# Kernel optimization log

Hardware: AMD Instinct MI355X
Metric: run time of the kernel (lower is better)

## Reference

```python
import jax, jax.numpy as jnp
import numpy as np
from jax import lax

D_MODEL = 1024
N_HEADS = 16
D_HEAD = 64
INNER = N_HEADS * D_HEAD
EPS = 1e-12  # F.normalize eps


def setup_inputs() -> dict:
    key = jax.random.key(0)
    ks = jax.random.split(key, 7)
    B, T = 4, 2048
    s = 1.0 / np.sqrt(D_MODEL)
    return {
        "x": jax.random.normal(ks[0], (B, T, D_MODEL), dtype=jnp.float32),
        "Wq": jax.random.normal(ks[1], (D_MODEL, INNER), dtype=jnp.float32) * s,
        "Wk": jax.random.normal(ks[2], (D_MODEL, INNER), dtype=jnp.float32) * s,
        "Wv": jax.random.normal(ks[3], (D_MODEL, INNER), dtype=jnp.float32) * s,
        "Wbeta": jax.random.normal(ks[4], (D_MODEL, N_HEADS), dtype=jnp.float32) * s,
        "b_beta": jax.random.normal(ks[5], (N_HEADS,), dtype=jnp.float32) * 0.01,
        "Wout": jax.random.normal(ks[6], (INNER, D_MODEL), dtype=jnp.float32) * (1.0 / np.sqrt(INNER)),
    }


def _delta_net(x, Wq, Wk, Wv, Wbeta, b_beta, Wout):
    B, T, _ = x.shape
    H, D = N_HEADS, D_HEAD
    Q = (x @ Wq).reshape(B, T, H, D)
    K = (x @ Wk).reshape(B, T, H, D)
    V = (x @ Wv).reshape(B, T, H, D)
    beta = jax.nn.sigmoid(x @ Wbeta + b_beta)  # (B,T,H)
    # L2-normalize keys along head dim (torch F.normalize semantics)
    K = K / jnp.maximum(jnp.linalg.norm(K, axis=-1, keepdims=True), EPS)

    # time-major for scan: (T,B,H,D) and (T,B,H)
    xs = (
        jnp.moveaxis(Q, 1, 0),
        jnp.moveaxis(K, 1, 0),
        jnp.moveaxis(V, 1, 0),
        jnp.moveaxis(beta, 1, 0),
    )

    def step(W, inp):
        q_t, k_t, v_t, b_t = inp
        pred = jnp.einsum('bhij,bhj->bhi', W, k_t)
        err = v_t - pred
        W_new = W + b_t[..., None, None] * jnp.einsum('bhi,bhj->bhij', err, k_t)
        o_t = jnp.einsum('bhij,bhj->bhi', W_new, q_t)
        return W_new, o_t

    W0 = jnp.zeros((B, H, D, D), dtype=x.dtype)
    _, O = lax.scan(step, W0, xs)  # O: (T,B,H,D)
    out = jnp.moveaxis(O, 0, 1).reshape(B, T, H * D)
    return out @ Wout


def reference(x, Wq, Wk, Wv, Wbeta, b_beta, Wout):
    return _delta_net(x, Wq, Wk, Wv, Wbeta, b_beta, Wout)
```

## Files before the change

### kernel.cpp

```cpp
#include <hip/hip_runtime.h>
#include <hip/hip_bf16.h>

#define BATCH 4
#define TSEQ 2048
#define DM 1024
#define NH 16
#define DH 64
#define MROWS (BATCH * TSEQ)
#define CHUNK 64
#define NCHUNK (TSEQ / CHUNK)

typedef __attribute__((ext_vector_type(8))) short bf16x8;
typedef __attribute__((ext_vector_type(4))) float f32x4;

#define GLOAD16(g, l)                                                        \
    __builtin_amdgcn_global_load_lds(                                        \
        (const __attribute__((address_space(1))) void*)(g),                  \
        (__attribute__((address_space(3))) void*)(l), 16, 0, 0)

__device__ __forceinline__ float ldf(const float* p) { return *p; }
__device__ __forceinline__ float ldf(const __hip_bfloat16* p) { return __bfloat162float(*p); }
__device__ __forceinline__ void stf(float* p, float v) { *p = v; }
__device__ __forceinline__ void stf(__hip_bfloat16* p, float v) { *p = __float2bfloat16(v); }

__device__ __forceinline__ int swz(int row, int cb) {
    return row * 128 + (cb ^ ((row & 7) << 4));
}
__device__ __forceinline__ bf16x8 ldfrag(const __hip_bfloat16* b, int rowblk, int kf, int lane) {
    const int row = rowblk * 16 + (lane & 15);
    const int cb = kf * 64 + ((lane >> 4) << 4);
    return *(const bf16x8*)((const char*)b + swz(row, cb));
}
__device__ __forceinline__ unsigned short bfbits(float f) {
    __hip_bfloat16 h = __float2bfloat16(f);
    return *(unsigned short*)&h;
}

template <int NSPLIT>
__global__ __launch_bounds__(256) void gemm_mfma(const __hip_bfloat16* __restrict__ Ah,
                                                 const __hip_bfloat16* __restrict__ BT,
                                                 float* __restrict__ Cf,
                                                 __hip_bfloat16* __restrict__ Qh,
                                                 int M, int N, int K) {
    __shared__ __align__(16) __hip_bfloat16 As[128 * 64];
    __shared__ __align__(16) __hip_bfloat16 Bs[128 * 64];
    const int tid = threadIdx.x;
    const int wave = tid >> 6;
    const int lane = tid & 63;
    const int wr = wave >> 1;
    const int wc = wave & 1;

    const int gx = gridDim.x;
    const int nwg = gx * gridDim.y;
    int bid = blockIdx.y * gx + blockIdx.x;
    bid = (bid & 7) * (nwg >> 3) + (bid >> 3);
    const int bx = bid % gx;
    const int by = bid / gx;
    const int wsel = (NSPLIT > 1) ? (bx >> 3) : 0;
    const __hip_bfloat16* BTp = BT + (size_t)wsel * DM * DM;
    const int rowBase = by * 128;
    const int colBase = ((NSPLIT > 1) ? (bx & 7) : bx) * 128;

    f32x4 acc[4][4] = {};

    const size_t Kz = (size_t)K;
    const int sg = (lane & 7) ^ (lane >> 3);
    const int rw0 = wave * 8 + (lane >> 3);

    for (int k0 = 0; k0 < K; k0 += 64) {
#pragma unroll
        for (int i = 0; i < 4; ++i) {
            const int row = rw0 + i * 32;
            GLOAD16(Ah + ((size_t)(rowBase + row) * Kz + k0 + sg * 8),
                    (char*)As + wave * 1024 + i * 4096);
            GLOAD16(BTp + ((size_t)(colBase + row) * Kz + k0 + sg * 8),
                    (char*)Bs + wave * 1024 + i * 4096);
        }
        __syncthreads();

#pragma unroll
        for (int kf = 0; kf < 2; ++kf) {
            bf16x8 af[4], bfr[4];
#pragma unroll
            for (int i = 0; i < 4; ++i) {
                const int ra = wr * 64 + i * 16 + (lane & 15);
                const int rb = wc * 64 + i * 16 + (lane & 15);
                const int slot = kf * 4 + (lane >> 4);
                const int cba = (slot ^ (lane & 7)) << 4;
                af[i] = *(const bf16x8*)((const char*)As + ra * 128 + cba);
                bfr[i] = *(const bf16x8*)((const char*)Bs + rb * 128 + cba);
            }
#pragma unroll
            for (int mi = 0; mi < 4; ++mi)
#pragma unroll
                for (int ni = 0; ni < 4; ++ni)
                    acc[mi][ni] = __builtin_amdgcn_mfma_f32_16x16x32_bf16(af[mi], bfr[ni],
                                                                          acc[mi][ni], 0, 0, 0);
        }
        __syncthreads();
    }

    if (NSPLIT > 1 && wsel == 0) {
#pragma unroll
        for (int mi = 0; mi < 4; ++mi)
#pragma unroll
            for (int ni = 0; ni < 4; ++ni) {
                const int col = colBase + wc * 64 + ni * 16 + (lane & 15);
#pragma unroll
                for (int r = 0; r < 4; ++r) {
                    const int row = rowBase + wr * 64 + mi * 16 + (lane >> 4) * 4 + r;
                    Qh[(size_t)row * N + col] = __float2bfloat16(acc[mi][ni][r]);
                }
            }
    } else {
        float* Cp = (NSPLIT > 1) ? (Cf + (size_t)(wsel - 1) * ((size_t)M * N)) : Cf;
#pragma unroll
        for (int mi = 0; mi < 4; ++mi)
#pragma unroll
            for (int ni = 0; ni < 4; ++ni) {
                const int col = colBase + wc * 64 + ni * 16 + (lane & 15);
#pragma unroll
                for (int r = 0; r < 4; ++r) {
                    const int row = rowBase + wr * 64 + mi * 16 + (lane >> 4) * 4 + r;
                    Cp[(size_t)row * N + col] = acc[mi][ni][r];
                }
            }
    }
}

__global__ __launch_bounds__(256) void conv_bf16(const float* __restrict__ in,
                                                 __hip_bfloat16* __restrict__ out, int n8) {
    const int i = blockIdx.x * 256 + threadIdx.x;
    if (i >= n8) return;
    const float4* p = (const float4*)in + (size_t)i * 2;
    float4 a = p[0], b = p[1];
    __hip_bfloat16 t[8] = {__float2bfloat16(a.x), __float2bfloat16(a.y),
                           __float2bfloat16(a.z), __float2bfloat16(a.w),
                           __float2bfloat16(b.x), __float2bfloat16(b.y),
                           __float2bfloat16(b.z), __float2bfloat16(b.w)};
    *(uint4*)(out + (size_t)i * 8) = *(const uint4*)t;
}

__global__ __launch_bounds__(256) void convT_bf16(const float* __restrict__ W,
                                                  __hip_bfloat16* __restrict__ WT) {
    __shared__ __hip_bfloat16 tile[64][65];
    const int tid = threadIdx.x;
    const int c = tid & 63;
    const int r4 = tid >> 6;
    const int kb = blockIdx.y * 64;
    const int nb = blockIdx.x * 64;
#pragma unroll
    for (int i = 0; i < 16; ++i) {
        const int r = r4 + i * 4;
        tile[r][c] = __float2bfloat16(W[(size_t)(kb + r) * DM + nb + c]);
    }
    __syncthreads();
#pragma unroll
    for (int i = 0; i < 16; ++i) {
        const int r = r4 + i * 4;
        WT[(size_t)(nb + r) * DM + kb + c] = tile[c][r];
    }
}

__global__ __launch_bounds__(256) void beta_kernel(const float* __restrict__ x,
                                                   const float* __restrict__ Wb,
                                                   const float* __restrict__ bb,
                                                   float* __restrict__ beta) {
    const int tid = threadIdx.x;
    const int h = tid % NH;
    const int rl = tid / NH;
    const int row = blockIdx.x * 16 + rl;
    const float* xr = x + (size_t)row * DM;
    float acc = 0.f;
#pragma unroll 8
    for (int k = 0; k < DM; ++k) acc += xr[k] * Wb[k * NH + h];
    acc += bb[h];
    beta[row * NH + h] = 1.f / (1.f + __expf(-acc));
}

__global__ __launch_bounds__(256) void delta_prepass(const float* __restrict__ K,
                                                     float* __restrict__ V,
                                                     const float* __restrict__ beta,
                                                     __hip_bfloat16* __restrict__ Wtt,
                                                     __hip_bfloat16* __restrict__ Kntt,
                                                     __hip_bfloat16* __restrict__ Knh) {
    const int chunk = blockIdx.x;
    const int bh = blockIdx.y;
    const int b = bh >> 4;
    const int h = bh & 15;
    const int tid = threadIdx.x;
    const int wave = tid >> 6;
    const int lane = tid & 63;
    const int lt = tid >> 2;
    const int j0 = (tid & 3) * 16;
    const int c0 = chunk * CHUNK;
    const size_t tileIdx = (size_t)bh * NCHUNK + chunk;

    __shared__ __align__(16) char smem_raw[17408 + 33792];
    float (*Am2)[68] = reinterpret_cast<float(*)[68]>(smem_raw);
    __hip_bfloat16* Knb = reinterpret_cast<__hip_bfloat16*>(smem_raw + 17408);
    float (*RT)[66] = reinterpret_cast<float(*)[66]>(smem_raw + 17408);
    __shared__ float sbeta[CHUNK];

    const size_t gstride = NH * DH;
    const size_t gbase = (size_t)b * TSEQ * gstride + (size_t)h * DH;
    const float* kp = K + gbase + (size_t)(c0 + lt) * gstride + j0;
    float* vp = V + gbase + (size_t)(c0 + lt) * gstride + j0;

    float4 k0 = ((const float4*)kp)[0];
    float4 k1 = ((const float4*)kp)[1];
    float4 k2 = ((const float4*)kp)[2];
    float4 k3 = ((const float4*)kp)[3];
    float ss = k0.x * k0.x + k0.y * k0.y + k0.z * k0.z + k0.w * k0.w +
               k1.x * k1.x + k1.y * k1.y + k1.z * k1.z + k1.w * k1.w +
               k2.x * k2.x + k2.y * k2.y + k2.z * k2.z + k2.w * k2.w +
               k3.x * k3.x + k3.y * k3.y + k3.z * k3.z + k3.w * k3.w;
    ss += __shfl_xor(ss, 1);
    ss += __shfl_xor(ss, 2);
    const float rn = 1.f / fmaxf(sqrtf(ss), 1e-12f);
    k0.x *= rn; k0.y *= rn; k0.z *= rn; k0.w *= rn;
    k1.x *= rn; k1.y *= rn; k1.z *= rn; k1.w *= rn;
    k2.x *= rn; k2.y *= rn; k2.z *= rn; k2.w *= rn;
    k3.x *= rn; k3.y *= rn; k3.z *= rn; k3.w *= rn;

    {
        __hip_bfloat16 t[16];
        const float kk[16] = {k0.x, k0.y, k0.z, k0.w, k1.x, k1.y, k1.z, k1.w,
                              k2.x, k2.y, k2.z, k2.w, k3.x, k3.y, k3.z, k3.w};
#pragma unroll
        for (int e = 0; e < 16; ++e) t[e] = __float2bfloat16(kk[e]);
        *(uint4*)((char*)Knb + swz(lt, j0 * 2)) = *(const uint4*)&t[0];
        *(uint4*)((char*)Knb + swz(lt, j0 * 2 + 16)) = *(const uint4*)&t[8];
        __hip_bfloat16* knh = Knh + gbase + (size_t)(c0 + lt) * gstride + j0;
        *(uint4*)knh = *(const uint4*)&t[0];
        *(uint4*)(knh + 8) = *(const uint4*)&t[8];
    }

    float4 v0 = ((const float4*)vp)[0];
    float4 v1 = ((const float4*)vp)[1];
    float4 v2 = ((const float4*)vp)[2];
    float4 v3 = ((const float4*)vp)[3];

    if (tid < CHUNK)
        sbeta[tid] = beta[((size_t)(b * TSEQ + c0 + tid)) * NH + h];
    __syncthreads();

    {
        f32x4 accA[4] = {};
#pragma unroll
        for (int kf = 0; kf < 2; ++kf) {
            bf16x8 ka = ldfrag(Knb, wave, kf, lane);
#pragma unroll
            for (int sb = 0; sb < 4; ++sb)
                accA[sb] = __builtin_amdgcn_mfma_f32_16x16x32_bf16(
                    ka, ldfrag(Knb, sb, kf, lane), accA[sb], 0, 0, 0);
        }
        float bt[4];
#pragma unroll
        for (int r = 0; r < 4; ++r) bt[r] = sbeta[16 * wave + (lane >> 4) * 4 + r];
#pragma unroll
        for (int sb = 0; sb < 4; ++sb)
#pragma unroll
            for (int r = 0; r < 4; ++r) {
                const int row = 16 * wave + (lane >> 4) * 4 + r;
                const int s = 16 * sb + (lane & 15);
                Am2[row][s] = (s < row) ? bt[r] * accA[sb][r] : 0.f;
            }
    }
    __syncthreads();

    {
        const int jr = tid >> 2;
        const int tq = (tid & 3) * 16;
        unsigned short pk[16];
#pragma unroll
        for (int i = 0; i < 16; ++i)
            pk[i] = *(const unsigned short*)((const char*)Knb + swz(tq + i, jr * 2));
        char* kt = (char*)Kntt + tileIdx * 8192;
        *(uint4*)(kt + swz(jr, tq * 2)) = *(const uint4*)&pk[0];
        *(uint4*)(kt + swz(jr, tq * 2 + 16)) = *(const uint4*)&pk[8];
    }
    __syncthreads();

    {
        const float bl = sbeta[lt];
        float vv[16] = {v0.x, v0.y, v0.z, v0.w, v1.x, v1.y, v1.z, v1.w,
                        v2.x, v2.y, v2.z, v2.w, v3.x, v3.y, v3.z, v3.w};
        float kk[16] = {k0.x, k0.y, k0.z, k0.w, k1.x, k1.y, k1.z, k1.w,
                        k2.x, k2.y, k2.z, k2.w, k3.x, k3.y, k3.z, k3.w};
#pragma unroll
        for (int e = 0; e < 16; ++e) {
            RT[j0 + e][lt] = bl * vv[e];
            RT[64 + j0 + e][lt] = bl * kk[e];
        }
    }
    __syncthreads();

    {
        const int c = tid >> 1;
        const int hh = tid & 1;
        float2 ra[16];
#pragma unroll
        for (int lp = 0; lp < 16; ++lp)
            ra[lp] = *(const float2*)&RT[c][4 * lp + 2 * hh];

#pragma unroll
        for (int tt = 0; tt < 16; ++tt) {
            const int t = 4 * tt;
            float2 mine = ra[tt];
            float2 other;
            other.x = __shfl_xor(mine.x, 1);
            other.y = __shfl_xor(mine.y, 1);
            const float r0 = hh ? other.x : mine.x;
            const float r1 = hh ? other.y : mine.y;
            const float r2 = hh ? mine.x : other.x;
            const float r3 = hh ? mine.y : other.y;
            const float4 q1 = *(const float4*)&Am2[t + 1][t];
            const float4 q2 = *(const float4*)&Am2[t + 2][t];
            const float4 q3 = *(const float4*)&Am2[t + 3][t];
            const float p0 = r0;
            const float p1 = r1 - q1.x * p0;
            const float p2 = r2 - q2.x * p0 - q2.y * p1;
            const float p3 = r3 - q3.x * p0 - q3.y * p1 - q3.z * p2;
            ra[tt] = hh ? make_float2(p2, p3) : make_float2(p0, p1);
#pragma unroll
            for (int lp = tt + 1; lp < 16; ++lp) {
                const int pr = 4 * lp + 2 * hh;
                const float4 ca = *(const float4*)&Am2[pr][t];
                const float4 cb = *(const float4*)&Am2[pr + 1][t];
                ra[lp].x -= ca.x * p0 + ca.y * p1 + ca.z * p2 + ca.w * p3;
                ra[lp].y -= cb.x * p0 + cb.y * p1 + cb.z * p2 + cb.w * p3;
            }
        }
#pragma unroll
        for (int lp = 0; lp < 16; ++lp)
            *(float2*)&RT[c][4 * lp + 2 * hh] = ra[lp];
    }
    __syncthreads();

    {
        float uu[16], ww[16];
#pragma unroll
        for (int e = 0; e < 16; ++e) {
            uu[e] = RT[j0 + e][lt];
            ww[e] = RT[64 + j0 + e][lt];
        }
#pragma unroll
        for (int q = 0; q < 4; ++q)
            ((float4*)vp)[q] = make_float4(uu[q * 4 + 0], uu[q * 4 + 1], uu[q * 4 + 2], uu[q * 4 + 3]);
        __hip_bfloat16 tw[16];
#pragma unroll
        for (int e = 0; e < 16; ++e) tw[e] = __float2bfloat16(ww[e]);
        char* wt = (char*)Wtt + tileIdx * 8192;
        *(uint4*)(wt + swz(lt, j0 * 2)) = *(const uint4*)&tw[0];
        *(uint4*)(wt + swz(lt, j0 * 2 + 16)) = *(const uint4*)&tw[8];
    }
}

__global__ __launch_bounds__(256) void scan_thin(const float* __restrict__ Ug,
                                                 const __hip_bfloat16* __restrict__ Wt,
                                                 const __hip_bfloat16* __restrict__ Kt,
                                                 __hip_bfloat16* __restrict__ Sg,
                                                 __hip_bfloat16* __restrict__ Utg) {
    const int bh = blockIdx.x;
    const int b = bh >> 4;
    const int h = bh & 15;
    const int tid = threadIdx.x;
    const int wave = tid >> 6;
    const int lane = tid & 63;
    const int srow = tid >> 2;
    const int sj0 = (tid & 3) * 16;

    __shared__ __align__(16) __hip_bfloat16 wb[2][64 * 64];
    __shared__ __align__(16) __hip_bfloat16 knT[2][64 * 64];
    __shared__ __align__(16) __hip_bfloat16 Sb[64 * 64];
    __shared__ __align__(16) __hip_bfloat16 Ut[64 * 64];

    const size_t gstride = NH * DH;
    const size_t gbase = (size_t)b * TSEQ * gstride + (size_t)h * DH;
    const size_t tileBase = (size_t)bh * NCHUNK;

    auto stage_tiles = [&](int buf, int c) {
        const char* wsrc = (const char*)Wt + (tileBase + c) * 8192 + wave * 1024 + lane * 16;
        const char* ksrc = (const char*)Kt + (tileBase + c) * 8192 + wave * 1024 + lane * 16;
#pragma unroll
        for (int q = 0; q < 2; ++q) {
            GLOAD16(wsrc + q * 4096, (char*)wb[buf] + wave * 1024 + q * 4096);
            GLOAD16(ksrc + q * 4096, (char*)knT[buf] + wave * 1024 + q * 4096);
        }
    };

    for (int i = tid; i < 512; i += 256) ((uint4*)Sb)[i] = make_uint4(0, 0, 0, 0);
    stage_tiles(0, 0);

    float up[4][4];
#pragma unroll
    for (int ib = 0; ib < 4; ++ib)
#pragma unroll
        for (int r = 0; r < 4; ++r) {
            const int t = 16 * wave + (lane >> 4) * 4 + r;
            up[ib][r] = Ug[gbase + (size_t)t * gstride + 16 * ib + (lane & 15)];
        }

    f32x4 Sreg[4] = {};
    __syncthreads();

    for (int c = 0; c < NCHUNK; ++c) {
        const int cur = c & 1;

        {
            uint4 a = *(const uint4*)((const char*)Sb + swz(srow, sj0 * 2));
            uint4 a2 = *(const uint4*)((const char*)Sb + swz(srow, sj0 * 2 + 16));
            __hip_bfloat16* gp = Sg + (tileBase + c) * 4096 + srow * 64 + sj0;
            *(uint4*)gp = a;
            *(uint4*)(gp + 8) = a2;
        }
        f32x4 accU[4] = {};
#pragma unroll
        for (int f = 0; f < 2; ++f) {
            bf16x8 wa = ldfrag(wb[cur], wave, f, lane);
#pragma unroll
            for (int ib = 0; ib < 4; ++ib)
                accU[ib] = __builtin_amdgcn_mfma_f32_16x16x32_bf16(
                    wa, ldfrag(Sb, ib, f, lane), accU[ib], 0, 0, 0);
        }
#pragma unroll
        for (int ib = 0; ib < 4; ++ib) {
            unsigned short pk[4];
#pragma unroll
            for (int r = 0; r < 4; ++r) pk[r] = bfbits(up[ib][r] - accU[ib][r]);
            const int irow = 16 * ib + (lane & 15);
            const int tcb = (16 * wave + (lane >> 4) * 4) * 2;
            *(unsigned long long*)((char*)Ut + swz(irow, tcb)) = *(const unsigned long long*)pk;
        }
        __syncthreads();

#pragma unroll
        for (int f = 0; f < 2; ++f) {
            bf16x8 ua = ldfrag(Ut, wave, f, lane);
#pragma unroll
            for (int jb = 0; jb < 4; ++jb)
                Sreg[jb] = __builtin_amdgcn_mfma_f32_16x16x32_bf16(
                    ua, ldfrag(knT[cur], jb, f, lane), Sreg[jb], 0, 0, 0);
        }
        {
            uint4 a = *(const uint4*)((const char*)Ut + swz(srow, sj0 * 2));
            uint4 a2 = *(const uint4*)((const char*)Ut + swz(srow, sj0 * 2 + 16));
            __hip_bfloat16* gp = Utg + (tileBase + c) * 4096 + srow * 64 + sj0;
            *(uint4*)gp = a;
            *(uint4*)(gp + 8) = a2;
        }
#pragma unroll
        for (int jb = 0; jb < 4; ++jb)
#pragma unroll
            for (int r = 0; r < 4; ++r) {
                const int irow = 16 * wave + (lane >> 4) * 4 + r;
                const int j = 16 * jb + (lane & 15);
                *(unsigned short*)((char*)Sb + swz(irow, j * 2)) = bfbits(Sreg[jb][r]);
            }
        if (c + 1 < NCHUNK) {
            stage_tiles(cur ^ 1, c + 1);
            const size_t nOff = (size_t)((c + 1) * CHUNK);
#pragma unroll
            for (int ib = 0; ib < 4; ++ib)
#pragma unroll
                for (int r = 0; r < 4; ++r) {
                    const int t = 16 * wave + (lane >> 4) * 4 + r;
                    up[ib][r] = Ug[gbase + (nOff + t) * gstride + 16 * ib + (lane & 15)];
                }
        }
        __syncthreads();
    }
}

__global__ __launch_bounds__(256) void delta_output(const __hip_bfloat16* __restrict__ Qh,
                                                    const __hip_bfloat16* __restrict__ Knh,
                                                    const __hip_bfloat16* __restrict__ Sg,
                                                    const __hip_bfloat16* __restrict__ Utg,
                                                    __hip_bfloat16* __restrict__ Ohg) {
    const int c = blockIdx.x;
    const int bh = blockIdx.y;
    const int b = bh >> 4;
    const int h = bh & 15;
    const int tid = threadIdx.x;
    const int wave = tid >> 6;
    const int lane = tid & 63;
    const int srow = tid >> 2;
    const int sj0 = (tid & 3) * 16;

    __shared__ __align__(16) __hip_bfloat16 Qb[64 * 64];
    __shared__ __align__(16) __hip_bfloat16 Knb[64 * 64];
    __shared__ __align__(16) __hip_bfloat16 Sbs[64 * 64];
    __shared__ __align__(16) __hip_bfloat16 Utb[64 * 64];
    __shared__ __align__(16) __hip_bfloat16 SSb[64 * 64];

    const size_t gstride = NH * DH;
    const size_t gbase = (size_t)b * TSEQ * gstride + (size_t)h * DH;
    const size_t cOff = (size_t)(c * CHUNK);
    const size_t tile = ((size_t)bh * NCHUNK + c) * 4096;

    {
        const uint4* qp = (const uint4*)(Qh + gbase + (cOff + srow) * gstride + sj0);
        const uint4* kp = (const uint4*)(Knh + gbase + (cOff + srow) * gstride + sj0);
        *(uint4*)((char*)Qb + swz(srow, sj0 * 2)) = qp[0];
        *(uint4*)((char*)Qb + swz(srow, sj0 * 2 + 16)) = qp[1];
        *(uint4*)((char*)Knb + swz(srow, sj0 * 2)) = kp[0];
        *(uint4*)((char*)Knb + swz(srow, sj0 * 2 + 16)) = kp[1];
        const uint4* sp = (const uint4*)(Sg + tile + srow * 64 + sj0);
        const uint4* upp = (const uint4*)(Utg + tile + srow * 64 + sj0);
        *(uint4*)((char*)Sbs + swz(srow, sj0 * 2)) = sp[0];
        *(uint4*)((char*)Sbs + swz(srow, sj0 * 2 + 16)) = sp[1];
        *(uint4*)((char*)Utb + swz(srow, sj0 * 2)) = upp[0];
        *(uint4*)((char*)Utb + swz(srow, sj0 * 2 + 16)) = upp[1];
    }
    __syncthreads();

    f32x4 ss[4] = {};
    f32x4 accO[4] = {};
#pragma unroll
    for (int f = 0; f < 2; ++f) {
        bf16x8 qa = ldfrag(Qb, wave, f, lane);
#pragma unroll
        for (int sb = 0; sb < 4; ++sb)
            ss[sb] = __builtin_amdgcn_mfma_f32_16x16x32_bf16(
                qa, ldfrag(Knb, sb, f, lane), ss[sb], 0, 0, 0);
#pragma unroll
        for (int ib = 0; ib < 4; ++ib)
            accO[ib] = __builtin_amdgcn_mfma_f32_16x16x32_bf16(
                qa, ldfrag(Sbs, ib, f, lane), accO[ib], 0, 0, 0);
    }
#pragma unroll
    for (int sb = 0; sb < 4; ++sb)
#pragma unroll
        for (int r = 0; r < 4; ++r) {
            const int t = 16 * wave + (lane >> 4) * 4 + r;
            const int s = 16 * sb + (lane & 15);
            const float v = (t >= s) ? ss[sb][r] : 0.f;
            *(unsigned short*)((char*)SSb + swz(t, s * 2)) = bfbits(v);
        }
    __syncthreads();

#pragma unroll
    for (int f = 0; f < 2; ++f) {
        bf16x8 sa = ldfrag(SSb, wave, f, lane);
#pragma unroll
        for (int ib = 0; ib < 4; ++ib)
            accO[ib] = __builtin_amdgcn_mfma_f32_16x16x32_bf16(
                sa, ldfrag(Utb, ib, f, lane), accO[ib], 0, 0, 0);
    }
#pragma unroll
    for (int ib = 0; ib < 4; ++ib)
#pragma unroll
        for (int r = 0; r < 4; ++r) {
            const int t = 16 * wave + (lane >> 4) * 4 + r;
            const int i = 16 * ib + (lane & 15);
            Ohg[gbase + (cOff + t) * gstride + i] = __float2bfloat16(accO[ib][r]);
        }
}

#define BM 64
#define BN 64
#define BK 16

template <typename TA, typename TC>
__global__ __launch_bounds__(256) void gemm_kernel(const TA* __restrict__ A,
                                                   const float* __restrict__ B,
                                                   TC* __restrict__ C,
                                                   int M, int N, int K) {
    __shared__ float As[BK][BM + 1];
    __shared__ float Bs[BK][BN + 1];
    const int tid = threadIdx.x;
    const int tr = tid / 16;
    const int tc = tid % 16;
    const int rowBase = blockIdx.y * BM;
    const int colBase = blockIdx.x * BN;

    float acc[4][4];
#pragma unroll
    for (int m = 0; m < 4; ++m)
#pragma unroll
        for (int n = 0; n < 4; ++n) acc[m][n] = 0.f;

    for (int k0 = 0; k0 < K; k0 += BK) {
#pragma unroll
        for (int i = tid; i < BM * BK; i += 256) {
            int r = i / BK, c = i % BK;
            As[c][r] = ldf(&A[(size_t)(rowBase + r) * K + k0 + c]);
        }
#pragma unroll
        for (int i = tid; i < BK * BN; i += 256) {
            int r = i / BN, c = i % BN;
            Bs[r][c] = B[(size_t)(k0 + r) * N + colBase + c];
        }
        __syncthreads();
#pragma unroll
        for (int kk = 0; kk < BK; ++kk) {
            float a[4], b[4];
#pragma unroll
            for (int m = 0; m < 4; ++m) a[m] = As[kk][tr * 4 + m];
#pragma unroll
            for (int n = 0; n < 4; ++n) b[n] = Bs[kk][tc * 4 + n];
#pragma unroll
            for (int m = 0; m < 4; ++m)
#pragma unroll
                for (int n = 0; n < 4; ++n) acc[m][n] += a[m] * b[n];
        }
        __syncthreads();
    }
#pragma unroll
    for (int m = 0; m < 4; ++m)
#pragma unroll
        for (int n = 0; n < 4; ++n)
            stf(&C[(size_t)(rowBase + tr * 4 + m) * N + colBase + tc * 4 + n], acc[m][n]);
}

template <typename TS>
__global__ __launch_bounds__(64) void scan_kernel(const TS* __restrict__ Q,
                                                  const TS* __restrict__ K,
                                                  const TS* __restrict__ V,
                                                  const float* __restrict__ beta,
                                                  float* __restrict__ O) {
    const int bh = blockIdx.x;
    const int b = bh >> 4;
    const int h = bh & 15;
    const int lane = threadIdx.x;

    float Wrow[64];
#pragma unroll
    for (int j = 0; j < 64; ++j) Wrow[j] = 0.f;

    __shared__ float sk[64];
    __shared__ float sq[64];

    size_t base = ((size_t)b * TSEQ) * (NH * DH) + h * DH + lane;
    int brow = b * TSEQ;

    for (int t = 0; t < TSEQ; ++t, base += NH * DH) {
        float k = ldf(&K[base]);
        float q = ldf(&Q[base]);
        float v = ldf(&V[base]);
        float be = beta[(size_t)(brow + t) * NH + h];

        float ss = k * k;
#pragma unroll
        for (int off = 32; off > 0; off >>= 1) ss += __shfl_xor(ss, off);
        k = k / fmaxf(sqrtf(ss), 1e-12f);

        sk[lane] = k;
        sq[lane] = q;
        __syncthreads();

        float p0 = 0.f, p1 = 0.f, p2 = 0.f, p3 = 0.f;
#pragma unroll
        for (int j = 0; j < 64; j += 4) {
            p0 += Wrow[j + 0] * sk[j + 0];
            p1 += Wrow[j + 1] * sk[j + 1];
            p2 += Wrow[j + 2] * sk[j + 2];
            p3 += Wrow[j + 3] * sk[j + 3];
        }
        const float bei = be * (v - ((p0 + p1) + (p2 + p3)));

        float o0 = 0.f, o1 = 0.f, o2 = 0.f, o3 = 0.f;
#pragma unroll
        for (int j = 0; j < 64; j += 4) {
            Wrow[j + 0] += bei * sk[j + 0]; o0 += Wrow[j + 0] * sq[j + 0];
            Wrow[j + 1] += bei * sk[j + 1]; o1 += Wrow[j + 1] * sq[j + 1];
            Wrow[j + 2] += bei * sk[j + 2]; o2 += Wrow[j + 2] * sq[j + 2];
            Wrow[j + 3] += bei * sk[j + 3]; o3 += Wrow[j + 3] * sq[j + 3];
        }
        O[base] = (o0 + o1) + (o2 + o3);
        __syncthreads();
    }
}

extern "C" void kernel_launch(void* const* d_in, const int* in_sizes, int n_in,
                              void* d_out, int out_size, void* d_ws, size_t ws_size,
                              hipStream_t stream) {
    const float* x     = (const float*)d_in[0];
    const float* Wq    = (const float*)d_in[1];
    const float* Wk    = (const float*)d_in[2];
    const float* Wv    = (const float*)d_in[3];
    const float* Wbeta = (const float*)d_in[4];
    const float* bbeta = (const float*)d_in[5];
    const float* Wout  = (const float*)d_in[6];
    float* out = (float*)d_out;

    const size_t projElems = (size_t)MROWS * DM;
    const size_t betaBytes = (size_t)MROWS * NH * 4;
    const size_t f32Bytes  = projElems * 4;
    const size_t bf16Bytes = projElems * 2;
    const size_t need_f32  = 4 * f32Bytes + betaBytes;

    char* ws = (char*)d_ws;
    size_t off = 0;
    auto alloc = [&](size_t bytes) {
        char* p = ws + off;
        off += (bytes + 255) & ~(size_t)255;
        return (void*)p;
    };

    if (ws_size >= need_f32) {
        float* Qf = (float*)alloc(f32Bytes);
        float* Kf = (float*)alloc(f32Bytes);
        float* Vf = (float*)alloc(f32Bytes);
        float* Wmf = (float*)alloc(f32Bytes);
        float* betaf = (float*)alloc(betaBytes);

        __hip_bfloat16* Qh  = (__hip_bfloat16*)Qf;
        __hip_bfloat16* Knh = (__hip_bfloat16*)((char*)Qf + bf16Bytes);

        __hip_bfloat16* xh  = (__hip_bfloat16*)Wmf;
        __hip_bfloat16* WqT = (__hip_bfloat16*)((char*)Wmf + bf16Bytes);
        __hip_bfloat16* WkT = WqT + (size_t)DM * DM;
        __hip_bfloat16* WvT = WkT + (size_t)DM * DM;

        const int n8 = (int)(projElems / 8);
        conv_bf16<<<dim3(n8 / 256), dim3(256), 0, stream>>>(x, xh, n8);
        convT_bf16<<<dim3(16, 16), dim3(256), 0, stream>>>(Wq, WqT);
        convT_bf16<<<dim3(16, 16), dim3(256), 0, stream>>>(Wk, WkT);
        convT_bf16<<<dim3(16, 16), dim3(256), 0, stream>>>(Wv, WvT);

        gemm_mfma<3><<<dim3(24, MROWS / 128), dim3(256), 0, stream>>>(xh, WqT, Kf, Qh,
                                                                      MROWS, DM, DM);
        beta_kernel<<<dim3(MROWS / 16), dim3(256), 0, stream>>>(x, Wbeta, bbeta, betaf);

        __hip_bfloat16* Wtt  = (__hip_bfloat16*)Wmf;
        __hip_bfloat16* Kntt = (__hip_bfloat16*)((char*)Wmf + bf16Bytes);
        delta_prepass<<<dim3(NCHUNK, BATCH * NH), dim3(256), 0, stream>>>(Kf, Vf, betaf,
                                                                          Wtt, Kntt, Knh);

        __hip_bfloat16* Sg  = (__hip_bfloat16*)d_out;
        __hip_bfloat16* Utg = Sg + (size_t)BATCH * NH * NCHUNK * 4096;
        scan_thin<<<dim3(BATCH * NH), dim3(256), 0, stream>>>(Vf, Wtt, Kntt, Sg, Utg);

        __hip_bfloat16* WoutT = (__hip_bfloat16*)Vf;
        __hip_bfloat16* Oh    = (__hip_bfloat16*)Wmf;
        convT_bf16<<<dim3(16, 16), dim3(256), 0, stream>>>(Wout, WoutT);
        delta_output<<<dim3(NCHUNK, BATCH * NH), dim3(256), 0, stream>>>(Qh, Knh, Sg, Utg, Oh);
        gemm_mfma<1><<<dim3(8, MROWS / 128), dim3(256), 0, stream>>>(Oh, WoutT, out, nullptr,
                                                                     MROWS, DM, DM);
    } else {
        __hip_bfloat16* Qh = (__hip_bfloat16*)alloc(bf16Bytes);
        __hip_bfloat16* Kh = (__hip_bfloat16*)alloc(bf16Bytes);
        __hip_bfloat16* Vh = (__hip_bfloat16*)alloc(bf16Bytes);
        float* betaf = (float*)alloc(betaBytes);
        float* Of = (float*)alloc(f32Bytes);

        const dim3 gemmGrid(DM / BN, MROWS / BM);
        gemm_kernel<float, __hip_bfloat16><<<gemmGrid, dim3(256), 0, stream>>>(x, Wq, Qh, MROWS, DM, DM);
        gemm_kernel<float, __hip_bfloat16><<<gemmGrid, dim3(256), 0, stream>>>(x, Wk, Kh, MROWS, DM, DM);
        gemm_kernel<float, __hip_bfloat16><<<gemmGrid, dim3(256), 0, stream>>>(x, Wv, Vh, MROWS, DM, DM);
        beta_kernel<<<dim3(MROWS / 16), dim3(256), 0, stream>>>(x, Wbeta, bbeta, betaf);
        scan_kernel<__hip_bfloat16><<<dim3(BATCH * NH), dim3(64), 0, stream>>>(Qh, Kh, Vh, betaf, Of);
        gemm_kernel<float, float><<<gemmGrid, dim3(256), 0, stream>>>(Of, Wout, out, MROWS, DM, DM);
    }
}
```

Before: 264.2 us.

## Fuse key L2-normalization into QKV GEMM epilogue and store K,V as bf16

The QKV GEMM epilogue now L2-normalizes K rows, using shuffle reductions across the 64-column head tile, and writes Q, normalized K and V directly as bf16 instead of writing K and V as fp32. The prepass reads bf16 K/V, no longer normalizes or re-emits K, and writes the updated U back as bf16. The scan reads U in bf16. This roughly halves the intermediate traffic for K, V and U and removes a redundant K write, at the cost of extra bf16 rounding of V and U before the scan.

```diff
diff --git a/kernel.cpp b/kernel.cpp
--- a/kernel.cpp
+++ b/kernel.cpp
@@ -40,7 +40,8 @@
 __global__ __launch_bounds__(256) void gemm_mfma(const __hip_bfloat16* __restrict__ Ah,
                                                  const __hip_bfloat16* __restrict__ BT,
                                                  float* __restrict__ Cf,
-                                                 __hip_bfloat16* __restrict__ Qh,
+                                                 __hip_bfloat16* __restrict__ QhBase,
+                                                 __hip_bfloat16* __restrict__ Vh,
                                                  int M, int N, int K) {
     __shared__ __align__(16) __hip_bfloat16 As[128 * 64];
     __shared__ __align__(16) __hip_bfloat16 Bs[128 * 64];
@@ -100,7 +101,25 @@
         __syncthreads();
     }
 
-    if (NSPLIT > 1 && wsel == 0) {
+    if (NSPLIT > 1) {
+        if (wsel == 1) {
+#pragma unroll
+            for (int mi = 0; mi < 4; ++mi)
+#pragma unroll
+                for (int r = 0; r < 4; ++r) {
+                    float ss = 0.f;
+#pragma unroll
+                    for (int ni = 0; ni < 4; ++ni) ss += acc[mi][ni][r] * acc[mi][ni][r];
+                    ss += __shfl_xor(ss, 1);
+                    ss += __shfl_xor(ss, 2);
+                    ss += __shfl_xor(ss, 4);
+                    ss += __shfl_xor(ss, 8);
+                    const float rn = 1.f / fmaxf(sqrtf(ss), 1e-12f);
+#pragma unroll
+                    for (int ni = 0; ni < 4; ++ni) acc[mi][ni][r] *= rn;
+                }
+        }
+        __hip_bfloat16* Op = (wsel == 2) ? Vh : (QhBase + (size_t)wsel * ((size_t)M * N));
 #pragma unroll
         for (int mi = 0; mi < 4; ++mi)
 #pragma unroll
@@ -109,11 +128,10 @@
 #pragma unroll
                 for (int r = 0; r < 4; ++r) {
                     const int row = rowBase + wr * 64 + mi * 16 + (lane >> 4) * 4 + r;
-                    Qh[(size_t)row * N + col] = __float2bfloat16(acc[mi][ni][r]);
+                    Op[(size_t)row * N + col] = __float2bfloat16(acc[mi][ni][r]);
                 }
             }
     } else {
-        float* Cp = (NSPLIT > 1) ? (Cf + (size_t)(wsel - 1) * ((size_t)M * N)) : Cf;
 #pragma unroll
         for (int mi = 0; mi < 4; ++mi)
 #pragma unroll
@@ -122,7 +140,7 @@
 #pragma unroll
                 for (int r = 0; r < 4; ++r) {
                     const int row = rowBase + wr * 64 + mi * 16 + (lane >> 4) * 4 + r;
-                    Cp[(size_t)row * N + col] = acc[mi][ni][r];
+                    Cf[(size_t)row * N + col] = acc[mi][ni][r];
                 }
             }
     }
@@ -178,12 +196,11 @@
     beta[row * NH + h] = 1.f / (1.f + __expf(-acc));
 }
 
-__global__ __launch_bounds__(256) void delta_prepass(const float* __restrict__ K,
-                                                     float* __restrict__ V,
+__global__ __launch_bounds__(256) void delta_prepass(const __hip_bfloat16* __restrict__ Knh,
+                                                     __hip_bfloat16* __restrict__ Vh,
                                                      const float* __restrict__ beta,
                                                      __hip_bfloat16* __restrict__ Wtt,
-                                                     __hip_bfloat16* __restrict__ Kntt,
-                                                     __hip_bfloat16* __restrict__ Knh) {
+                                                     __hip_bfloat16* __restrict__ Kntt) {
     const int chunk = blockIdx.x;
     const int bh = blockIdx.y;
     const int b = bh >> 4;
@@ -204,42 +221,30 @@
 
     const size_t gstride = NH * DH;
     const size_t gbase = (size_t)b * TSEQ * gstride + (size_t)h * DH;
-    const float* kp = K + gbase + (size_t)(c0 + lt) * gstride + j0;
-    float* vp = V + gbase + (size_t)(c0 + lt) * gstride + j0;
-
-    float4 k0 = ((const float4*)kp)[0];
-    float4 k1 = ((const float4*)kp)[1];
-    float4 k2 = ((const float4*)kp)[2];
-    float4 k3 = ((const float4*)kp)[3];
-    float ss = k0.x * k0.x + k0.y * k0.y + k0.z * k0.z + k0.w * k0.w +
-               k1.x * k1.x + k1.y * k1.y + k1.z * k1.z + k1.w * k1.w +
-               k2.x * k2.x + k2.y * k2.y + k2.z * k2.z + k2.w * k2.w +
-               k3.x * k3.x + k3.y * k3.y + k3.z * k3.z + k3.w * k3.w;
-    ss += __shfl_xor(ss, 1);
-    ss += __shfl_xor(ss, 2);
-    const float rn = 1.f / fmaxf(sqrtf(ss), 1e-12f);
-    k0.x *= rn; k0.y *= rn; k0.z *= rn; k0.w *= rn;
-    k1.x *= rn; k1.y *= rn; k1.z *= rn; k1.w *= rn;
-    k2.x *= rn; k2.y *= rn; k2.z *= rn; k2.w *= rn;
-    k3.x *= rn; k3.y *= rn; k3.z *= rn; k3.w *= rn;
-
+    const __hip_bfloat16* kp = Knh + gbase + (size_t)(c0 + lt) * gstride + j0;
+    __hip_bfloat16* vp = Vh + gbase + (size_t)(c0 + lt) * gstride + j0;
+
+    const uint4 kraw0 = ((const uint4*)kp)[0];
+    const uint4 kraw1 = ((const uint4*)kp)[1];
+    *(uint4*)((char*)Knb + swz(lt, j0 * 2)) = kraw0;
+    *(uint4*)((char*)Knb + swz(lt, j0 * 2 + 16)) = kraw1;
+    float kk[16], vv[16];
     {
-        __hip_bfloat16 t[16];
-        const float kk[16] = {k0.x, k0.y, k0.z, k0.w, k1.x, k1.y, k1.z, k1.w,
-                              k2.x, k2.y, k2.z, k2.w, k3.x, k3.y, k3.z, k3.w};
-#pragma unroll
-        for (int e = 0; e < 16; ++e) t[e] = __float2bfloat16(kk[e]);
-        *(uint4*)((char*)Knb + swz(lt, j0 * 2)) = *(const uint4*)&t[0];
-        *(uint4*)((char*)Knb + swz(lt, j0 * 2 + 16)) = *(const uint4*)&t[8];
-        __hip_bfloat16* knh = Knh + gbase + (size_t)(c0 + lt) * gstride + j0;
-        *(uint4*)knh = *(const uint4*)&t[0];
-        *(uint4*)(knh + 8) = *(const uint4*)&t[8];
-    }
-
-    float4 v0 = ((const float4*)vp)[0];
-    float4 v1 = ((const float4*)vp)[1];
-    float4 v2 = ((const float4*)vp)[2];
-    float4 v3 = ((const float4*)vp)[3];
+        const __hip_bfloat16* kb16 = (const __hip_bfloat16*)&kraw0;
+#pragma unroll
+        for (int e = 0; e < 8; ++e) kk[e] = __bfloat162float(kb16[e]);
+        kb16 = (const __hip_bfloat16*)&kraw1;
+#pragma unroll
+        for (int e = 0; e < 8; ++e) kk[8 + e] = __bfloat162float(kb16[e]);
+        const uint4 vraw0 = ((const uint4*)vp)[0];
+        const uint4 vraw1 = ((const uint4*)vp)[1];
+        const __hip_bfloat16* vb16 = (const __hip_bfloat16*)&vraw0;
+#pragma unroll
+        for (int e = 0; e < 8; ++e) vv[e] = __bfloat162float(vb16[e]);
+        vb16 = (const __hip_bfloat16*)&vraw1;
+#pragma unroll
+        for (int e = 0; e < 8; ++e) vv[8 + e] = __bfloat162float(vb16[e]);
+    }
 
     if (tid < CHUNK)
         sbeta[tid] = beta[((size_t)(b * TSEQ + c0 + tid)) * NH + h];
@@ -284,10 +289,6 @@
 
     {
         const float bl = sbeta[lt];
-        float vv[16] = {v0.x, v0.y, v0.z, v0.w, v1.x, v1.y, v1.z, v1.w,
-                        v2.x, v2.y, v2.z, v2.w, v3.x, v3.y, v3.z, v3.w};
-        float kk[16] = {k0.x, k0.y, k0.z, k0.w, k1.x, k1.y, k1.z, k1.w,
-                        k2.x, k2.y, k2.z, k2.w, k3.x, k3.y, k3.z, k3.w};
 #pragma unroll
         for (int e = 0; e < 16; ++e) {
             RT[j0 + e][lt] = bl * vv[e];
@@ -345,19 +346,21 @@
             uu[e] = RT[j0 + e][lt];
             ww[e] = RT[64 + j0 + e][lt];
         }
-#pragma unroll
-        for (int q = 0; q < 4; ++q)
-            ((float4*)vp)[q] = make_float4(uu[q * 4 + 0], uu[q * 4 + 1], uu[q * 4 + 2], uu[q * 4 + 3]);
-        __hip_bfloat16 tw[16];
-#pragma unroll
-        for (int e = 0; e < 16; ++e) tw[e] = __float2bfloat16(ww[e]);
+        __hip_bfloat16 tu[16], tw[16];
+#pragma unroll
+        for (int e = 0; e < 16; ++e) {
+            tu[e] = __float2bfloat16(uu[e]);
+            tw[e] = __float2bfloat16(ww[e]);
+        }
+        *(uint4*)vp = *(const uint4*)&tu[0];
+        *(uint4*)(vp + 8) = *(const uint4*)&tu[8];
         char* wt = (char*)Wtt + tileIdx * 8192;
         *(uint4*)(wt + swz(lt, j0 * 2)) = *(const uint4*)&tw[0];
         *(uint4*)(wt + swz(lt, j0 * 2 + 16)) = *(const uint4*)&tw[8];
     }
 }
 
-__global__ __launch_bounds__(256) void scan_thin(const float* __restrict__ Ug,
+__global__ __launch_bounds__(256) void scan_thin(const __hip_bfloat16* __restrict__ Ug,
                                                  const __hip_bfloat16* __restrict__ Wt,
                                                  const __hip_bfloat16* __restrict__ Kt,
                                                  __hip_bfloat16* __restrict__ Sg,
@@ -399,7 +402,7 @@
 #pragma unroll
         for (int r = 0; r < 4; ++r) {
             const int t = 16 * wave + (lane >> 4) * 4 + r;
-            up[ib][r] = Ug[gbase + (size_t)t * gstride + 16 * ib + (lane & 15)];
+            up[ib][r] = __bfloat162float(Ug[gbase + (size_t)t * gstride + 16 * ib + (lane & 15)]);
         }
 
     f32x4 Sreg[4] = {};
@@ -466,7 +469,8 @@
 #pragma unroll
                 for (int r = 0; r < 4; ++r) {
                     const int t = 16 * wave + (lane >> 4) * 4 + r;
-                    up[ib][r] = Ug[gbase + (nOff + t) * gstride + 16 * ib + (lane & 15)];
+                    up[ib][r] =
+                        __bfloat162float(Ug[gbase + (nOff + t) * gstride + 16 * ib + (lane & 15)]);
                 }
         }
         __syncthreads();
@@ -705,9 +709,12 @@
         float* Vf = (float*)alloc(f32Bytes);
         float* Wmf = (float*)alloc(f32Bytes);
         float* betaf = (float*)alloc(betaBytes);
-
-        __hip_bfloat16* Qh  = (__hip_bfloat16*)Qf;
-        __hip_bfloat16* Knh = (__hip_bfloat16*)((char*)Qf + bf16Bytes);
+        (void)Vf;
+
+        __hip_bfloat16* Qh    = (__hip_bfloat16*)Qf;
+        __hip_bfloat16* Knh   = Qh + projElems;
+        __hip_bfloat16* Vh    = (__hip_bfloat16*)Kf;
+        __hip_bfloat16* WoutT = (__hip_bfloat16*)((char*)Kf + bf16Bytes);
 
         __hip_bfloat16* xh  = (__hip_bfloat16*)Wmf;
         __hip_bfloat16* WqT = (__hip_bfloat16*)((char*)Wmf + bf16Bytes);
@@ -720,25 +727,24 @@
         convT_bf16<<<dim3(16, 16), dim3(256), 0, stream>>>(Wk, WkT);
         convT_bf16<<<dim3(16, 16), dim3(256), 0, stream>>>(Wv, WvT);
 
-        gemm_mfma<3><<<dim3(24, MROWS / 128), dim3(256), 0, stream>>>(xh, WqT, Kf, Qh,
+        gemm_mfma<3><<<dim3(24, MROWS / 128), dim3(256), 0, stream>>>(xh, WqT, nullptr, Qh, Vh,
                                                                       MROWS, DM, DM);
         beta_kernel<<<dim3(MROWS / 16), dim3(256), 0, stream>>>(x, Wbeta, bbeta, betaf);
 
         __hip_bfloat16* Wtt  = (__hip_bfloat16*)Wmf;
         __hip_bfloat16* Kntt = (__hip_bfloat16*)((char*)Wmf + bf16Bytes);
-        delta_prepass<<<dim3(NCHUNK, BATCH * NH), dim3(256), 0, stream>>>(Kf, Vf, betaf,
-                                                                          Wtt, Kntt, Knh);
+        delta_prepass<<<dim3(NCHUNK, BATCH * NH), dim3(256), 0, stream>>>(Knh, Vh, betaf,
+                                                                          Wtt, Kntt);
 
         __hip_bfloat16* Sg  = (__hip_bfloat16*)d_out;
         __hip_bfloat16* Utg = Sg + (size_t)BATCH * NH * NCHUNK * 4096;
-        scan_thin<<<dim3(BATCH * NH), dim3(256), 0, stream>>>(Vf, Wtt, Kntt, Sg, Utg);
-
-        __hip_bfloat16* WoutT = (__hip_bfloat16*)Vf;
-        __hip_bfloat16* Oh    = (__hip_bfloat16*)Wmf;
+        scan_thin<<<dim3(BATCH * NH), dim3(256), 0, stream>>>(Vh, Wtt, Kntt, Sg, Utg);
+
+        __hip_bfloat16* Oh = (__hip_bfloat16*)Wmf;
         convT_bf16<<<dim3(16, 16), dim3(256), 0, stream>>>(Wout, WoutT);
         delta_output<<<dim3(NCHUNK, BATCH * NH), dim3(256), 0, stream>>>(Qh, Knh, Sg, Utg, Oh);
         gemm_mfma<1><<<dim3(8, MROWS / 128), dim3(256), 0, stream>>>(Oh, WoutT, out, nullptr,
-                                                                     MROWS, DM, DM);
+                                                                     nullptr, MROWS, DM, DM);
     } else {
         __hip_bfloat16* Qh = (__hip_bfloat16*)alloc(bf16Bytes);
         __hip_bfloat16* Kh = (__hip_bfloat16*)alloc(bf16Bytes);
```

Measured after the change: 292.5 us. +10.7%, slower.
